# Optimization experiments

Hardware: AMD Instinct MI355X
Metric: run time of the kernel (lower is better)

The kernel has to match this reference:

```python
import jax, jax.numpy as jnp
import numpy as np
import math

BASE_RES = 16
MAX_RES = 2048
LEVELS = 16
FEAT_DIM = 2
LOG_B = math.log(MAX_RES / BASE_RES) / (LEVELS - 1)  # per-level log scale


def setup_inputs() -> dict:
    key = jax.random.key(0)
    k1, k2 = jax.random.split(key)
    B = 1048576
    positions = jax.random.uniform(k1, (B, 3), dtype=jnp.float32)
    total = MAX_RES * MAX_RES * 3 * FEAT_DIM
    # torch.nn.init.uniform_ -> U[0,1)
    plane_table = jax.random.uniform(k2, (total,), dtype=jnp.float32)
    return {"positions": positions, "plane_table": plane_table}


def _encode(positions, plane_table):
    B = positions.shape[0]
    dtype = positions.dtype
    # planes: (xy, yz, zx) -> [B, 3 planes, 2 coords]
    x, y, z = positions[:, 0], positions[:, 1], positions[:, 2]
    xyz6 = jnp.stack([x, y, y, z, z, x], axis=1).reshape(B, 3, 2)
    planes = plane_table.reshape(3, MAX_RES * MAX_RES, FEAT_DIM)
    plane_ids = jnp.arange(3)  # [3]
    outs = []
    for level in range(LEVELS):
        scale = BASE_RES * math.exp(level * LOG_B) - 1.0
        res = int(math.ceil(scale)) + 1  # grid_resolution
        pos = xyz6 * (res - 1) + 0.5            # [B,3,2]
        pg = jnp.floor(pos)
        frac = pos - pg                          # fractional part
        pg = pg.astype(jnp.int32)
        local = jnp.zeros((B, 3, FEAT_DIM), dtype)
        for idx in range(4):  # 4 bilinear corners
            w = jnp.ones((B, 3), dtype)
            coords = []
            for d in range(2):
                if idx & (1 << d):
                    coords.append(pg[..., d] + 1)
                    w = w * frac[..., d]
                else:
                    coords.append(pg[..., d])
                    w = w * (1.0 - frac[..., d])
            c = jnp.stack(coords, axis=-1).astype(dtype)  # [B,3,2]
            # remap corner from level grid to the max_res storage grid (truncating cast)
            c_ori = (c / res * (MAX_RES - 1)).astype(jnp.int32)
            index = c_ori[..., 0] + c_ori[..., 1] * MAX_RES  # [B,3] flat plane index
            feats = planes[plane_ids[None, :], index]        # [B,3,FEAT_DIM] gather
            local = local + w[..., None] * feats
        # cross-plane product
        outs.append(local[:, 0] * local[:, 1] * local[:, 2])  # [B,FEAT_DIM]
    out = jnp.stack(outs, axis=2)  # [B, FEAT_DIM, LEVELS]; sn = j*LEVELS + level
    return out.reshape(B, FEAT_DIM * LEVELS)


def reference(positions, plane_table):
    return _encode(positions, plane_table)
```

## Files before the change

### kernel.cpp

```cpp
#include <hip/hip_runtime.h>
#include <math.h>

#define LEVELS 16
#define MAX_RES 2048
#define NCELL_BITS 5
#define NCELLS (1 << (3 * NCELL_BITS))

typedef float nfloat4 __attribute__((ext_vector_type(4)));

struct ResParams { int res[LEVELS]; };


__global__ __launch_bounds__(256) void zero_hist(unsigned int* hist) {
  int i = blockIdx.x * 256 + threadIdx.x;
  if (i < NCELLS) hist[i] = 0u;
}

__device__ __forceinline__ unsigned int morton5(int cx, int cy, int cz) {
  unsigned int k = 0;
  #pragma unroll
  for (int b = 0; b < NCELL_BITS; ++b)
    k |= (((cx >> b) & 1) << (3 * b)) | (((cy >> b) & 1) << (3 * b + 1)) |
         (((cz >> b) & 1) << (3 * b + 2));
  return k;
}

__device__ __forceinline__ unsigned int cell_of(float x, float y, float z) {
  int cx = min(31, max(0, (int)(x * 32.0f)));
  int cy = min(31, max(0, (int)(y * 32.0f)));
  int cz = min(31, max(0, (int)(z * 32.0f)));
  return morton5(cx, cy, cz);
}

__global__ __launch_bounds__(256) void keys_hist(const float* __restrict__ pos,
                                                 unsigned int* __restrict__ hist, int B) {
  int i = blockIdx.x * 256 + threadIdx.x;
  if (i >= B) return;
  atomicAdd(&hist[cell_of(pos[i*3], pos[i*3+1], pos[i*3+2])], 1u);
}

__global__ __launch_bounds__(1024) void scan_kernel(const unsigned int* __restrict__ hist,
                                                    unsigned int* __restrict__ offs) {
  __shared__ unsigned int part[1024];
  const int SEG = NCELLS / 1024;
  int t = threadIdx.x;
  int base = t * SEG;
  unsigned int s = 0;
  #pragma unroll
  for (int j = 0; j < SEG; ++j) s += hist[base + j];
  part[t] = s;
  __syncthreads();
  for (int off = 1; off < 1024; off <<= 1) {
    unsigned int v = (t >= off) ? part[t - off] : 0u;
    __syncthreads();
    part[t] += v;
    __syncthreads();
  }
  unsigned int run = part[t] - s;
  #pragma unroll
  for (int j = 0; j < SEG; ++j) {
    unsigned int c = hist[base + j];
    offs[base + j] = run;
    run += c;
  }
}

__global__ __launch_bounds__(256) void scatter_kernel(const float* __restrict__ pos,
                                                      unsigned int* __restrict__ offs,
                                                      nfloat4* __restrict__ sorted, int B) {
  int i = blockIdx.x * 256 + threadIdx.x;
  if (i >= B) return;
  float x = pos[i*3], y = pos[i*3+1], z = pos[i*3+2];
  unsigned int slot = atomicAdd(&offs[cell_of(x, y, z)], 1u);
  nfloat4 v = {x, y, z, __int_as_float(i)};
  sorted[slot] = v;
}


__global__ __launch_bounds__(256) void triplane_main(
    const nfloat4* __restrict__ sorted,
    const float* __restrict__ table,
    float* __restrict__ out,
    ResParams P, int B, int nwg)
{
  int wg = blockIdx.x;
  int q = nwg >> 3, r = nwg & 7;
  int xcd = wg & 7, idx = wg >> 3;
  int swz = (xcd < r) ? xcd * (q + 1) + idx : r * (q + 1) + (xcd - r) * q + idx;
  int t = swz * 256 + (int)threadIdx.x;
  if (t >= B) return;

  nfloat4 s = sorted[t];
  float x = s.x, y = s.y, z = s.z;
  int orig = __float_as_int(s.w);

  float uarr[3] = {x, y, z};
  float varr[3] = {y, z, x};

  float o0[LEVELS], o1[LEVELS];

  #pragma unroll
  for (int l = 0; l < LEVELS; ++l) {
    const int   res   = P.res[l];
    const float resm1 = (float)(res - 1);
    const float fres  = (float)res;

    float prod0 = 1.0f, prod1 = 1.0f;

    #pragma unroll
    for (int p = 0; p < 3; ++p) {
      float pu = __fadd_rn(__fmul_rn(uarr[p], resm1), 0.5f);
      float pv = __fadd_rn(__fmul_rn(varr[p], resm1), 0.5f);
      float gu = floorf(pu), gv = floorf(pv);
      float fu = __fsub_rn(pu, gu);
      float fv = __fsub_rn(pv, gv);
      float gu1 = __fadd_rn(gu, 1.0f);
      float gv1 = __fadd_rn(gv, 1.0f);

      int cou0 = (int)(__fmul_rn(__fdiv_rn(gu,  fres), 2047.0f));
      int cou1 = (int)(__fmul_rn(__fdiv_rn(gu1, fres), 2047.0f));
      int cov0 = (int)(__fmul_rn(__fdiv_rn(gv,  fres), 2047.0f));
      int cov1 = (int)(__fmul_rn(__fdiv_rn(gv1, fres), 2047.0f));

      const float* plane = table + (size_t)p * (MAX_RES * MAX_RES * 2);

      const float2 f00 = *reinterpret_cast<const float2*>(plane + (size_t)(cou0 + (cov0 << 11)) * 2);
      const float2 f10 = *reinterpret_cast<const float2*>(plane + (size_t)(cou1 + (cov0 << 11)) * 2);
      const float2 f01 = *reinterpret_cast<const float2*>(plane + (size_t)(cou0 + (cov1 << 11)) * 2);
      const float2 f11 = *reinterpret_cast<const float2*>(plane + (size_t)(cou1 + (cov1 << 11)) * 2);

      float w00 = (1.0f - fu) * (1.0f - fv);
      float w10 = fu * (1.0f - fv);
      float w01 = (1.0f - fu) * fv;
      float w11 = fu * fv;

      float a0 = 0.0f, a1 = 0.0f;
      a0 += w00 * f00.x;  a1 += w00 * f00.y;
      a0 += w10 * f10.x;  a1 += w10 * f10.y;
      a0 += w01 * f01.x;  a1 += w01 * f01.y;
      a0 += w11 * f11.x;  a1 += w11 * f11.y;

      prod0 *= a0;
      prod1 *= a1;
    }

    o0[l] = prod0;
    o1[l] = prod1;
  }

  nfloat4* base = reinterpret_cast<nfloat4*>(out + (size_t)orig * 32);
  #pragma unroll
  for (int k = 0; k < 4; ++k) {
    nfloat4 v0 = {o0[k*4+0], o0[k*4+1], o0[k*4+2], o0[k*4+3]};
    nfloat4 v1 = {o1[k*4+0], o1[k*4+1], o1[k*4+2], o1[k*4+3]};
    base[k] = v0;
    base[4 + k] = v1;
  }
}

extern "C" void kernel_launch(void* const* d_in, const int* in_sizes, int n_in,
                              void* d_out, int out_size, void* d_ws, size_t ws_size,
                              hipStream_t stream) {
  const float* positions = (const float*)d_in[0];
  const float* table     = (const float*)d_in[1];
  float* out             = (float*)d_out;
  int B = in_sizes[0] / 3;

  ResParams P;
  const double LOG_B = log(2048.0 / 16.0) / (double)(LEVELS - 1);
  for (int l = 0; l < LEVELS; ++l) {
    double scale = 16.0 * exp((double)l * LOG_B) - 1.0;
    P.res[l] = (int)ceil(scale) + 1;
  }

  int nwg = (B + 255) / 256;

  size_t off_hist   = 0;
  size_t off_offs   = off_hist + (size_t)NCELLS * 4;
  size_t off_sorted = off_offs + (size_t)NCELLS * 4;
  size_t need       = off_sorted + (size_t)B * 16;

  if (ws_size >= need) {
    unsigned int* hist = (unsigned int*)((char*)d_ws + off_hist);
    unsigned int* offs = (unsigned int*)((char*)d_ws + off_offs);
    nfloat4*      srt  = (nfloat4*)((char*)d_ws + off_sorted);

    hipLaunchKernelGGL(zero_hist, dim3((NCELLS + 255) / 256), dim3(256), 0, stream, hist);
    hipLaunchKernelGGL(keys_hist, dim3(nwg), dim3(256), 0, stream, positions, hist, B);
    hipLaunchKernelGGL(scan_kernel, dim3(1), dim3(1024), 0, stream, hist, offs);
    hipLaunchKernelGGL(scatter_kernel, dim3(nwg), dim3(256), 0, stream, positions, offs, srt, B);
    hipLaunchKernelGGL(triplane_main, dim3(nwg), dim3(256), 0, stream,
                       srt, table, out, P, B, nwg);
  }
}
```

Before: 444.8 us.

## Gather mid-level grid features into compact per-level tables before sampling

Adds a pre-pass that, for levels 9-13, copies the remapped storage-grid entries into a dense per-level (res+1)^2 table per plane. The main kernel then indexes these compact tables directly instead of doing four divisions and scattered gathers into the 2048x2048 plane. The aim is better cache locality and fewer divides for those levels. The cost is an extra kernel launch plus the memory traffic of building the tables on every call, and the new path depends on the workspace being large enough.

New measurement: 466.8 us. 4.9% more time.

```diff
diff --git a/kernel.cpp b/kernel.cpp
--- a/kernel.cpp
+++ b/kernel.cpp
@@ -5,10 +5,16 @@
 #define MAX_RES 2048
 #define NCELL_BITS 5
 #define NCELLS (1 << (3 * NCELL_BITS))
+#define LC_LO 9
+#define LC_HI 13
 
 typedef float nfloat4 __attribute__((ext_vector_type(4)));
 
-struct ResParams { int res[LEVELS]; };
+struct ResParams {
+  int res[LEVELS];
+  int coff[LEVELS];
+  int S[LEVELS];
+};
 
 
 __global__ __launch_bounds__(256) void zero_hist(unsigned int* hist) {
@@ -76,10 +82,32 @@
   sorted[slot] = v;
 }
 
-
+__global__ __launch_bounds__(256) void build_compact(const float* __restrict__ table,
+                                                     float2* __restrict__ compact,
+                                                     ResParams P) {
+  int l = LC_LO + blockIdx.y;
+  int S = P.S[l];
+  int e = blockIdx.x * 256 + threadIdx.x;
+  if (e >= 3 * S) return;
+  int res = P.res[l];
+  int W = res + 1;
+  int p = e / S;
+  int rem = e - p * S;
+  int v = rem / W;
+  int u = rem - v * W;
+  const float fres = (float)res;
+  int cu = (int)(__fmul_rn(__fdiv_rn((float)u, fres), 2047.0f));
+  int cv = (int)(__fmul_rn(__fdiv_rn((float)v, fres), 2047.0f));
+  const float* plane = table + (size_t)p * (MAX_RES * MAX_RES * 2);
+  compact[P.coff[l] + e] = *reinterpret_cast<const float2*>(plane + (size_t)(cu + (cv << 11)) * 2);
+}
+
+
+template <bool USE_COMPACT>
 __global__ __launch_bounds__(256) void triplane_main(
     const nfloat4* __restrict__ sorted,
     const float* __restrict__ table,
+    const float2* __restrict__ compact,
     float* __restrict__ out,
     ResParams P, int B, int nwg)
 {
@@ -104,6 +132,7 @@
     const int   res   = P.res[l];
     const float resm1 = (float)(res - 1);
     const float fres  = (float)res;
+    const bool  cpath = USE_COMPACT && (l >= LC_LO && l <= LC_HI);
 
     float prod0 = 1.0f, prod1 = 1.0f;
 
@@ -114,20 +143,33 @@
       float gu = floorf(pu), gv = floorf(pv);
       float fu = __fsub_rn(pu, gu);
       float fv = __fsub_rn(pv, gv);
-      float gu1 = __fadd_rn(gu, 1.0f);
-      float gv1 = __fadd_rn(gv, 1.0f);
-
-      int cou0 = (int)(__fmul_rn(__fdiv_rn(gu,  fres), 2047.0f));
-      int cou1 = (int)(__fmul_rn(__fdiv_rn(gu1, fres), 2047.0f));
-      int cov0 = (int)(__fmul_rn(__fdiv_rn(gv,  fres), 2047.0f));
-      int cov1 = (int)(__fmul_rn(__fdiv_rn(gv1, fres), 2047.0f));
-
-      const float* plane = table + (size_t)p * (MAX_RES * MAX_RES * 2);
-
-      const float2 f00 = *reinterpret_cast<const float2*>(plane + (size_t)(cou0 + (cov0 << 11)) * 2);
-      const float2 f10 = *reinterpret_cast<const float2*>(plane + (size_t)(cou1 + (cov0 << 11)) * 2);
-      const float2 f01 = *reinterpret_cast<const float2*>(plane + (size_t)(cou0 + (cov1 << 11)) * 2);
-      const float2 f11 = *reinterpret_cast<const float2*>(plane + (size_t)(cou1 + (cov1 << 11)) * 2);
+
+      float2 f00, f10, f01, f11;
+
+      if (cpath) {
+        int iu = (int)gu, iv = (int)gv;
+        int W = res + 1;
+        const float2* lv = compact + (P.coff[l] + p * P.S[l]);
+        int i0 = iv * W + iu;
+        int i1 = i0 + W;
+        f00 = lv[i0];
+        f10 = lv[i0 + 1];
+        f01 = lv[i1];
+        f11 = lv[i1 + 1];
+      } else {
+        float gu1 = __fadd_rn(gu, 1.0f);
+        float gv1 = __fadd_rn(gv, 1.0f);
+        int cou0 = (int)(__fmul_rn(__fdiv_rn(gu,  fres), 2047.0f));
+        int cou1 = (int)(__fmul_rn(__fdiv_rn(gu1, fres), 2047.0f));
+        int cov0 = (int)(__fmul_rn(__fdiv_rn(gv,  fres), 2047.0f));
+        int cov1 = (int)(__fmul_rn(__fdiv_rn(gv1, fres), 2047.0f));
+
+        const float* plane = table + (size_t)p * (MAX_RES * MAX_RES * 2);
+        f00 = *reinterpret_cast<const float2*>(plane + (size_t)(cou0 + (cov0 << 11)) * 2);
+        f10 = *reinterpret_cast<const float2*>(plane + (size_t)(cou1 + (cov0 << 11)) * 2);
+        f01 = *reinterpret_cast<const float2*>(plane + (size_t)(cou0 + (cov1 << 11)) * 2);
+        f11 = *reinterpret_cast<const float2*>(plane + (size_t)(cou1 + (cov1 << 11)) * 2);
+      }
 
       float w00 = (1.0f - fu) * (1.0f - fv);
       float w10 = fu * (1.0f - fv);
@@ -168,28 +210,49 @@
 
   ResParams P;
   const double LOG_B = log(2048.0 / 16.0) / (double)(LEVELS - 1);
+  int runoff = 0, Smax = 0;
   for (int l = 0; l < LEVELS; ++l) {
     double scale = 16.0 * exp((double)l * LOG_B) - 1.0;
     P.res[l] = (int)ceil(scale) + 1;
+    P.coff[l] = 0; P.S[l] = 0;
+  }
+  for (int l = LC_LO; l <= LC_HI; ++l) {
+    int W = P.res[l] + 1;
+    P.S[l] = W * W;
+    P.coff[l] = runoff;
+    runoff += 3 * P.S[l];
+    if (P.S[l] > Smax) Smax = P.S[l];
   }
 
   int nwg = (B + 255) / 256;
 
-  size_t off_hist   = 0;
-  size_t off_offs   = off_hist + (size_t)NCELLS * 4;
-  size_t off_sorted = off_offs + (size_t)NCELLS * 4;
-  size_t need       = off_sorted + (size_t)B * 16;
-
-  if (ws_size >= need) {
-    unsigned int* hist = (unsigned int*)((char*)d_ws + off_hist);
-    unsigned int* offs = (unsigned int*)((char*)d_ws + off_offs);
-    nfloat4*      srt  = (nfloat4*)((char*)d_ws + off_sorted);
-
-    hipLaunchKernelGGL(zero_hist, dim3((NCELLS + 255) / 256), dim3(256), 0, stream, hist);
-    hipLaunchKernelGGL(keys_hist, dim3(nwg), dim3(256), 0, stream, positions, hist, B);
-    hipLaunchKernelGGL(scan_kernel, dim3(1), dim3(1024), 0, stream, hist, offs);
-    hipLaunchKernelGGL(scatter_kernel, dim3(nwg), dim3(256), 0, stream, positions, offs, srt, B);
-    hipLaunchKernelGGL(triplane_main, dim3(nwg), dim3(256), 0, stream,
-                       srt, table, out, P, B, nwg);
-  }
-}
+  size_t off_hist    = 0;
+  size_t off_offs    = off_hist + (size_t)NCELLS * 4;
+  size_t off_sorted  = off_offs + (size_t)NCELLS * 4;
+  size_t off_compact = off_sorted + (size_t)B * 16;
+  size_t need_sort   = off_compact;
+  size_t need_all    = off_compact + (size_t)runoff * 8;
+
+  if (ws_size < need_sort) return;
+
+  unsigned int* hist = (unsigned int*)((char*)d_ws + off_hist);
+  unsigned int* offs = (unsigned int*)((char*)d_ws + off_offs);
+  nfloat4*      srt  = (nfloat4*)((char*)d_ws + off_sorted);
+  float2*       cmp  = (float2*)((char*)d_ws + off_compact);
+
+  hipLaunchKernelGGL(zero_hist, dim3((NCELLS + 255) / 256), dim3(256), 0, stream, hist);
+  hipLaunchKernelGGL(keys_hist, dim3(nwg), dim3(256), 0, stream, positions, hist, B);
+  hipLaunchKernelGGL(scan_kernel, dim3(1), dim3(1024), 0, stream, hist, offs);
+  hipLaunchKernelGGL(scatter_kernel, dim3(nwg), dim3(256), 0, stream, positions, offs, srt, B);
+
+  if (ws_size >= need_all) {
+    int nx = (3 * Smax + 255) / 256;
+    int ny = LC_HI - LC_LO + 1;
+    hipLaunchKernelGGL(build_compact, dim3(nx, ny), dim3(256), 0, stream, table, cmp, P);
+    hipLaunchKernelGGL((triplane_main<true>), dim3(nwg), dim3(256), 0, stream,
+                       srt, table, cmp, out, P, B, nwg);
+  } else {
+    hipLaunchKernelGGL((triplane_main<false>), dim3(nwg), dim3(256), 0, stream,
+                       srt, table, cmp, out, P, B, nwg);
+  }
+}
```
